# Kernel optimization log

Hardware: AMD Instinct MI355X
Metric: run time of the kernel (lower is better)

Reference implementation:

```python
import jax, jax.numpy as jnp
import numpy as np

INNER = 256   # inner_channel
NODES = 64    # nodes_num (prototypes)
EM_NUM = 3
DIAG_C = 128  # hardcoded diag_channel in FullyConnectGCLayer


def setup_inputs() -> dict:
    key = jax.random.key(0)
    ks = jax.random.split(key, 16)
    b, c, w, h = 4, 1024, 64, 64
    f32 = jnp.float32
    d = {}
    d["x"] = jax.random.normal(ks[0], (b, c, w, h), f32)
    # Conv2d weights re-initialized to N(0, 0.001) in Intra_graph.__init__
    d["W_in"] = 0.001 * jax.random.normal(ks[1], (INNER, c), f32)
    d["b_in"] = jnp.zeros((INNER,), f32)
    d["multi_proto"] = 0.001 * jax.random.normal(ks[2], (1, INNER, NODES), f32)
    d["pi0"] = jnp.ones((1, NODES), f32) / NODES
    # Conv1d layers keep default kaiming-uniform-ish init
    lim = 1.0 / np.sqrt(INNER)
    d["W_adj"] = jax.random.uniform(ks[3], (DIAG_C, INNER), f32, -lim, lim)
    d["b_adj"] = jax.random.uniform(ks[4], (DIAG_C,), f32, -lim, lim)
    d["W_diag"] = jax.random.uniform(ks[5], (DIAG_C, INNER), f32, -lim, lim)
    d["b_diag"] = jax.random.uniform(ks[6], (DIAG_C,), f32, -lim, lim)
    d["gcn_weight"] = 0.01 * jax.random.normal(ks[7], (INNER, INNER), f32)
    d["W_out"] = 0.001 * jax.random.normal(ks[8], (c, INNER), f32)
    d["b_out"] = jnp.zeros((c,), f32)
    d["gamma"] = jnp.ones((c,), f32)
    d["beta"] = jnp.zeros((c,), f32)
    d["W_out2"] = 0.001 * jax.random.normal(ks[9], (c, INNER), f32)
    d["b_out2"] = jnp.zeros((c,), f32)
    d["gamma2"] = jnp.ones((c,), f32)
    d["beta2"] = jnp.zeros((c,), f32)
    d["flag"] = 0
    return d


def _bn(y, g, bt):
    # BatchNorm2d in training mode: batch stats over (N,H,W), biased var, eps=1e-5
    m = jnp.mean(y, (0, 2, 3), keepdims=True)
    v = jnp.var(y, (0, 2, 3), keepdims=True)
    return (y - m) * jax.lax.rsqrt(v + 1e-5) * g[None, :, None, None] + bt[None, :, None, None]


def _forward(x, W_in, b_in, multi_proto, pi0, W_adj, b_adj, W_diag, b_diag,
             gcn_weight, W_out, b_out, gamma, beta, W_out2, b_out2, gamma2, beta2):
    b, c, w, h = x.shape
    wh = w * h
    x1 = (jnp.einsum('oi,bihw->bohw', W_in, x) + b_in[None, :, None, None]).reshape(b, INNER, wh)
    # ---- EM soft-clustering loop (runs under no_grad in torch) ----
    x1s = jax.lax.stop_gradient(x1)
    mu = jnp.broadcast_to(multi_proto, (b, INNER, NODES))
    pi = jnp.broadcast_to(pi0[None, :, :], (b, 1, NODES))
    for _ in range(EM_NUM):
        lik = jnp.einsum('bcm,bcn->bmn', x1s, mu)              # [b, wh, n]
        lik = jnp.exp(lik - jnp.max(lik, 2, keepdims=True))
        post = lik * pi
        post = post / (1e-18 + jnp.sum(post, 2, keepdims=True))
        prob = post / (1e-18 + jnp.sum(post, 1, keepdims=True))
        mu = jnp.einsum('bcm,bmn->bcn', x1s, prob)
        pi = jnp.sum(post, 1, keepdims=True) / wh
    post = jax.lax.stop_gradient(post)
    prob = jax.lax.stop_gradient(prob)
    # ---- aggregate to prototypes (grad flows through x1 only) ----
    x2 = jnp.einsum('bcm,bmn->bcn', x1, prob)                   # [b, inner, n]
    # ---- branch 2: scatter back, conv, bn ----
    x4 = jnp.einsum('bcn,bmn->bcm', x2, post).reshape(b, INNER, w, h)
    x4 = _bn(jnp.einsum('oi,bihw->bohw', W_out2, x4) + b_out2[None, :, None, None], gamma2, beta2)
    output2 = jax.nn.relu(jax.nn.relu(x4) + x)
    # ---- FullyConnectGCLayer on x2 ----
    xd = jnp.einsum('oi,bin->bon', W_diag, x2) + b_diag[None, :, None]
    dvec = jax.nn.sigmoid(jnp.mean(xd, 2))                      # [b, 128]
    xa = jnp.einsum('oi,bin->bon', W_adj, x2) + b_adj[None, :, None]  # [b, 128, n]
    # sigmoid(diag(d)) has 0.5 off-diagonal, sigmoid(d) on diagonal:
    # xa^T S xa = 0.5 * (1^T xa)^T (1^T xa) + xa^T diag(sig(d)-0.5) xa
    u = jnp.sum(xa, 1)                                          # [b, n]
    A = 0.5 * u[:, :, None] * u[:, None, :] + jnp.einsum('bcn,bc,bcm->bnm', xa, dvec - 0.5, xa)
    A = jax.nn.relu(A) + jnp.eye(NODES, dtype=x.dtype)[None]
    deg = jax.lax.stop_gradient(jnp.sum(A, 1) ** -0.5)          # no_grad degree, [b, n]
    A = deg[:, :, None] * A * deg[:, None, :]
    gout = jnp.einsum('oi,bin->bon', gcn_weight, jnp.einsum('bcn,bnm->bcm', x2, A))
    x2g = jax.nn.relu(gout) + x2                                # res_connect
    # ---- branch 1: scatter back, conv, bn ----
    x3 = jnp.einsum('bcn,bmn->bcm', x2g, post).reshape(b, INNER, w, h)
    x3 = _bn(jnp.einsum('oi,bihw->bohw', W_out, x3) + b_out[None, :, None, None], gamma, beta)
    output = jax.nn.relu(jax.nn.relu(x3) + x)
    return output, output2


def reference(x, W_in, b_in, multi_proto, pi0, W_adj, b_adj, W_diag, b_diag,
              gcn_weight, W_out, b_out, gamma, beta, W_out2, b_out2, gamma2, beta2, flag):
    # flag only gates a buffer EMA update (no effect on forward outputs)
    return _forward(x, W_in, b_in, multi_proto, pi0, W_adj, b_adj, W_diag, b_diag,
                    gcn_weight, W_out, b_out, gamma, beta, W_out2, b_out2, gamma2, beta2)
```

## Files before the change

kernel.cpp:

```cpp
#include <hip/hip_runtime.h>
#include <math.h>


typedef unsigned short u16;
typedef short s16x8 __attribute__((ext_vector_type(8)));
typedef float f32x4 __attribute__((ext_vector_type(4)));

constexpr int BB  = 4;
constexpr int CH  = 1024;
constexpr int IN  = 256;
constexpr int ND  = 64;
constexpr int WH  = 4096;
constexpr int DCN = 128;
constexpr size_t TOT = (size_t)BB * CH * WH;

__device__ inline u16 f2bf(float f) {
  unsigned u = __float_as_uint(f);
  return (u16)((u + 0x7fffu + ((u >> 16) & 1u)) >> 16);
}
__device__ inline s16x8 ld8(const u16* p) { return *(const s16x8*)p; }
#define MFMA16(a, b, c) __builtin_amdgcn_mfma_f32_16x16x32_bf16(a, b, c, 0, 0, 0)

__global__ void k_init(const float* __restrict__ Win, const float* __restrict__ mp,
                       const float* __restrict__ pi0, u16* __restrict__ Winb,
                       u16* __restrict__ mu_t, float* __restrict__ piw,
                       float* __restrict__ sp) {
  int idx = blockIdx.x * 256 + threadIdx.x;
  if (idx < IN * CH) { Winb[idx] = f2bf(Win[idx]); return; }
  int j = idx - IN * CH;
  if (j < BB * ND * IN) {
    int bb = j >> 14, n = (j >> 8) & 63, c = j & 255;
    mu_t[((size_t)(bb * ND + n)) * IN + c] = f2bf(mp[c * ND + n]);
    return;
  }
  j -= BB * ND * IN;
  if (j < BB * ND) { piw[j] = pi0[j & 63]; return; }
  j -= BB * ND;
  if (j < 3 * BB * ND) sp[j] = 0.f;
}

__global__ __launch_bounds__(512) void k_x1(
    const float* __restrict__ x, const u16* __restrict__ Winb,
    const float* __restrict__ bin, u16* __restrict__ x1, u16* __restrict__ x1t) {
  __shared__ u16 lt[64][40];
  const int t = threadIdx.x, w = t >> 6, lr = t & 15, lg = (t >> 4) & 3;
  const int wc = w & 3, wm = w >> 2;
  const int m0 = blockIdx.x * 64, b = blockIdx.y;
  const int si = t >> 4, sm = (t & 15) * 4;
  const float* xb = x + (size_t)b * CH * WH + m0 + sm;
  f32x4 acc[4][2];
#pragma unroll
  for (int i = 0; i < 4; ++i)
#pragma unroll
    for (int j = 0; j < 2; ++j) acc[i][j] = (f32x4){0.f, 0.f, 0.f, 0.f};
  const u16* wp = Winb + (size_t)(wc * 64 + lr) * CH + lg * 8;

  float4 nxt = *(const float4*)&xb[(size_t)si * WH];
  for (int k0 = 0; k0 < CH; k0 += 32) {
    float4 cur = nxt;
    __syncthreads();
    lt[sm + 0][si] = f2bf(cur.x); lt[sm + 1][si] = f2bf(cur.y);
    lt[sm + 2][si] = f2bf(cur.z); lt[sm + 3][si] = f2bf(cur.w);
    if (k0 + 32 < CH) nxt = *(const float4*)&xb[(size_t)(k0 + 32 + si) * WH];
    __syncthreads();
    s16x8 af[4], bf[2];
#pragma unroll
    for (int i = 0; i < 4; ++i) af[i] = ld8(wp + (size_t)i * 16 * CH + k0);
#pragma unroll
    for (int j = 0; j < 2; ++j) bf[j] = *(const s16x8*)&lt[wm * 32 + j * 16 + lr][lg * 8];
#pragma unroll
    for (int i = 0; i < 4; ++i)
#pragma unroll
      for (int j = 0; j < 2; ++j) acc[i][j] = MFMA16(af[i], bf[j], acc[i][j]);
  }
#pragma unroll
  for (int i = 0; i < 4; ++i) {
    const int cb = wc * 64 + i * 16 + lg * 4;
    const float4 bi = *(const float4*)&bin[cb];
    const float bia[4] = {bi.x, bi.y, bi.z, bi.w};
#pragma unroll
    for (int j = 0; j < 2; ++j) {
      const int m = m0 + wm * 32 + j * 16 + lr;
      float v[4];
#pragma unroll
      for (int r = 0; r < 4; ++r) v[r] = acc[i][j][r] + bia[r];
      ushort4 o;
      o.x = f2bf(v[0]); o.y = f2bf(v[1]); o.z = f2bf(v[2]); o.w = f2bf(v[3]);
      *(ushort4*)&x1t[((size_t)b * WH + m) * IN + cb] = o;
#pragma unroll
      for (int r = 0; r < 4; ++r)
        x1[((size_t)b * IN + cb + r) * WH + m] = f2bf(v[r]);
    }
  }
}

__global__ __launch_bounds__(256) void k_em(
    const u16* __restrict__ x1, const u16* __restrict__ x1t,
    const u16* __restrict__ mu_t, const float* __restrict__ piw,
    float* __restrict__ sp, u16* __restrict__ pmn,
    float* __restrict__ mup, float* __restrict__ gp, int doG) {
  __shared__ u16 ptl[64][72];
  const int t = threadIdx.x, w = t >> 6, lr = t & 15, lg = (t >> 4) & 3;
  const int mch = blockIdx.x, b = blockIdx.y;
  {
    f32x4 acc[4];
#pragma unroll
    for (int f = 0; f < 4; ++f) acc[f] = (f32x4){0.f, 0.f, 0.f, 0.f};
    const u16* ap = x1t + ((size_t)b * WH + mch * 64 + w * 16 + lr) * IN + lg * 8;
    const u16* bp = mu_t + ((size_t)b * ND + lr) * IN + lg * 8;
#pragma unroll
    for (int k0 = 0; k0 < IN; k0 += 32) {
      s16x8 a = ld8(ap + k0);
#pragma unroll
      for (int f = 0; f < 4; ++f)
        acc[f] = MFMA16(a, ld8(bp + f * 16 * IN + k0), acc[f]);
    }
    float pi_[4], spart[4] = {0.f, 0.f, 0.f, 0.f};
#pragma unroll
    for (int f = 0; f < 4; ++f) pi_[f] = piw[b * ND + f * 16 + lr];
#pragma unroll
    for (int r = 0; r < 4; ++r) {
      float v0 = acc[0][r], v1 = acc[1][r], v2 = acc[2][r], v3 = acc[3][r];
      float mx = fmaxf(fmaxf(v0, v1), fmaxf(v2, v3));
      mx = fmaxf(mx, __shfl_xor(mx, 1)); mx = fmaxf(mx, __shfl_xor(mx, 2));
      mx = fmaxf(mx, __shfl_xor(mx, 4)); mx = fmaxf(mx, __shfl_xor(mx, 8));
      float e0 = __expf(v0 - mx) * pi_[0], e1 = __expf(v1 - mx) * pi_[1];
      float e2 = __expf(v2 - mx) * pi_[2], e3 = __expf(v3 - mx) * pi_[3];
      float s = e0 + e1 + e2 + e3;
      s += __shfl_xor(s, 1); s += __shfl_xor(s, 2);
      s += __shfl_xor(s, 4); s += __shfl_xor(s, 8);
      const float inv = 1.f / (1e-18f + s);
      e0 *= inv; e1 *= inv; e2 *= inv; e3 *= inv;
      const int mloc = w * 16 + lg * 4 + r;
      const size_t gbase = ((size_t)b * WH + mch * 64 + mloc) * ND + lr;
      u16 q0 = f2bf(e0), q1 = f2bf(e1), q2 = f2bf(e2), q3 = f2bf(e3);
      pmn[gbase + 0]  = q0; pmn[gbase + 16] = q1;
      pmn[gbase + 32] = q2; pmn[gbase + 48] = q3;
      ptl[0 + lr][mloc]  = q0; ptl[16 + lr][mloc] = q1;
      ptl[32 + lr][mloc] = q2; ptl[48 + lr][mloc] = q3;
      spart[0] += e0; spart[1] += e1; spart[2] += e2; spart[3] += e3;
    }
#pragma unroll
    for (int f = 0; f < 4; ++f) {
      spart[f] += __shfl_xor(spart[f], 16);
      spart[f] += __shfl_xor(spart[f], 32);
    }
    if (((t >> 4) & 3) == 0) {
#pragma unroll
      for (int f = 0; f < 4; ++f)
        atomicAdd(&sp[b * ND + f * 16 + lr], spart[f]);
    }
  }
  __syncthreads();
  {
    f32x4 acc[4][4];
#pragma unroll
    for (int i = 0; i < 4; ++i)
#pragma unroll
      for (int j = 0; j < 4; ++j) acc[i][j] = (f32x4){0.f, 0.f, 0.f, 0.f};
    const u16* ap = x1 + ((size_t)b * IN + w * 64 + lr) * WH + mch * 64 + lg * 8;
#pragma unroll
    for (int ks = 0; ks < 2; ++ks) {
      s16x8 af[4], bf[4];
#pragma unroll
      for (int i = 0; i < 4; ++i) af[i] = ld8(ap + (size_t)i * 16 * WH + ks * 32);
#pragma unroll
      for (int j = 0; j < 4; ++j)
        bf[j] = *(const s16x8*)&ptl[j * 16 + lr][ks * 32 + lg * 8];
#pragma unroll
      for (int i = 0; i < 4; ++i)
#pragma unroll
        for (int j = 0; j < 4; ++j) acc[i][j] = MFMA16(af[i], bf[j], acc[i][j]);
    }
    float* mo = mup + ((size_t)mch * BB + b) * (IN * ND);
#pragma unroll
    for (int i = 0; i < 4; ++i)
#pragma unroll
      for (int j = 0; j < 4; ++j)
#pragma unroll
        for (int r = 0; r < 4; ++r) {
          const int c = w * 64 + i * 16 + lg * 4 + r, n = j * 16 + lr;
          mo[c * ND + n] = acc[i][j][r];
        }
  }
  if (doG) {
    f32x4 acc[4];
#pragma unroll
    for (int j = 0; j < 4; ++j) acc[j] = (f32x4){0.f, 0.f, 0.f, 0.f};
#pragma unroll
    for (int ks = 0; ks < 2; ++ks) {
      s16x8 a = *(const s16x8*)&ptl[w * 16 + lr][ks * 32 + lg * 8];
#pragma unroll
      for (int j = 0; j < 4; ++j) {
        s16x8 bq = *(const s16x8*)&ptl[j * 16 + lr][ks * 32 + lg * 8];
        acc[j] = MFMA16(a, bq, acc[j]);
      }
    }
    float* go = gp + ((size_t)mch * BB + b) * (ND * ND);
#pragma unroll
    for (int j = 0; j < 4; ++j)
#pragma unroll
      for (int r = 0; r < 4; ++r) {
        const int n1 = w * 16 + lg * 4 + r, n2 = j * 16 + lr;
        go[n1 * ND + n2] = acc[j][r];
      }
  }
}

__global__ void k_mu_red(const float* __restrict__ mup, const float* __restrict__ spb,
                         float* __restrict__ piw, float* __restrict__ mu,
                         u16* __restrict__ mu_t, const float* __restrict__ gp,
                         float* __restrict__ G, int doG) {
  const int idx = blockIdx.x * 256 + threadIdx.x;
  const int bb = idx >> 14, c = (idx >> 6) & 255, n = idx & 63;
  float s = 0.f;
#pragma unroll 8
  for (int ch = 0; ch < 64; ++ch)
    s += mup[((size_t)ch * BB + bb) * (IN * ND) + (idx & 16383)];
  const float v = s / (1e-18f + spb[bb * ND + n]);
  mu[idx] = v;
  mu_t[((size_t)(bb * ND + n)) * IN + c] = f2bf(v);
  if (idx < BB * ND) piw[idx] = spb[idx] * (1.f / (float)WH);
  if (doG && idx < BB * ND * ND) {
    float g = 0.f;
#pragma unroll 8
    for (int ch = 0; ch < 64; ++ch) g += gp[(size_t)ch * (BB * ND * ND) + idx];
    G[idx] = g;
  }
}

__global__ __launch_bounds__(256) void k_gcA(
    const float* __restrict__ mu, const float* __restrict__ gw,
    const float* __restrict__ Wa, const float* __restrict__ ba,
    const float* __restrict__ Wd, const float* __restrict__ bd,
    float* __restrict__ qbuf, float* __restrict__ xabuf, float* __restrict__ dv) {
  __shared__ float sx2[IN * ND];
  __shared__ float srm[IN];
  const int t = threadIdx.x, blk = blockIdx.x, b = blockIdx.y;
  if (blk < 6) {
    const float* src = mu + (size_t)b * IN * ND;
#pragma unroll
    for (int q4 = 0; q4 < 16; ++q4)
      *(float4*)&sx2[q4 * 1024 + t * 4] = *(const float4*)&src[q4 * 1024 + t * 4];
    __syncthreads();
    const int rg = t >> 4, cg = t & 15;
    const float* W = (blk < 4) ? gw + (size_t)(blk * 64 + rg * 4) * IN
                               : Wa + (size_t)((blk - 4) * 64 + rg * 4) * IN;
    float acc[4][4] = {};
    for (int i4 = 0; i4 < 64; ++i4) {
      float4 xv[4];
#pragma unroll
      for (int e = 0; e < 4; ++e)
        xv[e] = *(const float4*)&sx2[(i4 * 4 + e) * 64 + cg * 4];
#pragma unroll
      for (int rr = 0; rr < 4; ++rr) {
        const float4 w4 = *(const float4*)&W[(size_t)rr * IN + i4 * 4];
        acc[rr][0] += w4.x * xv[0].x + w4.y * xv[1].x + w4.z * xv[2].x + w4.w * xv[3].x;
        acc[rr][1] += w4.x * xv[0].y + w4.y * xv[1].y + w4.z * xv[2].y + w4.w * xv[3].y;
        acc[rr][2] += w4.x * xv[0].z + w4.y * xv[1].z + w4.z * xv[2].z + w4.w * xv[3].z;
        acc[rr][3] += w4.x * xv[0].w + w4.y * xv[1].w + w4.z * xv[2].w + w4.w * xv[3].w;
      }
    }
    if (blk < 4) {
      float* dst = qbuf + (size_t)b * IN * ND + (size_t)(blk * 64 + rg * 4) * ND + cg * 4;
#pragma unroll
      for (int rr = 0; rr < 4; ++rr)
        *(float4*)&dst[(size_t)rr * ND] =
            make_float4(acc[rr][0], acc[rr][1], acc[rr][2], acc[rr][3]);
    } else {
      const int xr = (blk - 4) * 64 + rg * 4;
      float* dst = xabuf + (size_t)b * DCN * ND + (size_t)xr * ND + cg * 4;
#pragma unroll
      for (int rr = 0; rr < 4; ++rr) {
        const float bv = ba[xr + rr];
        *(float4*)&dst[(size_t)rr * ND] =
            make_float4(acc[rr][0] + bv, acc[rr][1] + bv, acc[rr][2] + bv, acc[rr][3] + bv);
      }
    }
  } else {
    {
      const float* row = mu + (size_t)b * IN * ND + (size_t)t * ND;
      float s = 0.f;
#pragma unroll
      for (int n4 = 0; n4 < 16; ++n4) {
        float4 v = *(const float4*)&row[n4 * 4];
        s += v.x + v.y + v.z + v.w;
      }
      srm[t] = s * (1.f / ND);
    }
    __syncthreads();
    if (t < DCN) {
      float a = 0.f;
#pragma unroll
      for (int i4 = 0; i4 < 64; ++i4) {
        float4 w4 = *(const float4*)&Wd[(size_t)t * IN + i4 * 4];
        float4 r4 = *(const float4*)&srm[i4 * 4];
        a += w4.x * r4.x + w4.y * r4.y + w4.z * r4.z + w4.w * r4.w;
      }
      a += bd[t];
      dv[b * DCN + t] = 1.f / (1.f + __expf(-a)) - 0.5f;
    }
  }
}

__global__ __launch_bounds__(256) void k_gcB(
    const float* __restrict__ xabuf, const float* __restrict__ dv,
    float* __restrict__ ahat) {
  __shared__ float sxa[DCN * ND];
  __shared__ float sdv[DCN];
  __shared__ float su[ND];
  __shared__ float sdeg[ND];
  __shared__ float sA[ND * 65];
  const int t = threadIdx.x, b = blockIdx.x;
  const float* src = xabuf + (size_t)b * DCN * ND;
#pragma unroll
  for (int q4 = 0; q4 < 8; ++q4)
    *(float4*)&sxa[q4 * 1024 + t * 4] = *(const float4*)&src[q4 * 1024 + t * 4];
  if (t < DCN) sdv[t] = dv[b * DCN + t];
  __syncthreads();
  if (t < ND) {
    float s = 0.f;
    for (int dc = 0; dc < DCN; ++dc) s += sxa[dc * ND + t];
    su[t] = s;
  }
  __syncthreads();
  {
    const int n1g = t >> 4, n2g = t & 15;
    float acc[4][4] = {};
    for (int dc = 0; dc < DCN; ++dc) {
      const float dvv = sdv[dc];
      float4 v1 = *(const float4*)&sxa[dc * ND + n1g * 4];
      const float4 v2 = *(const float4*)&sxa[dc * ND + n2g * 4];
      v1.x *= dvv; v1.y *= dvv; v1.z *= dvv; v1.w *= dvv;
      acc[0][0] += v1.x * v2.x; acc[0][1] += v1.x * v2.y;
      acc[0][2] += v1.x * v2.z; acc[0][3] += v1.x * v2.w;
      acc[1][0] += v1.y * v2.x; acc[1][1] += v1.y * v2.y;
      acc[1][2] += v1.y * v2.z; acc[1][3] += v1.y * v2.w;
      acc[2][0] += v1.z * v2.x; acc[2][1] += v1.z * v2.y;
      acc[2][2] += v1.z * v2.z; acc[2][3] += v1.z * v2.w;
      acc[3][0] += v1.w * v2.x; acc[3][1] += v1.w * v2.y;
      acc[3][2] += v1.w * v2.z; acc[3][3] += v1.w * v2.w;
    }
#pragma unroll
    for (int i = 0; i < 4; ++i) {
      const int n1 = n1g * 4 + i;
      const float u1 = su[n1];
#pragma unroll
      for (int j = 0; j < 4; ++j) {
        const int n2 = n2g * 4 + j;
        const float v = acc[i][j] + 0.5f * u1 * su[n2];
        sA[n1 * 65 + n2] = fmaxf(v, 0.f) + (n1 == n2 ? 1.f : 0.f);
      }
    }
  }
  __syncthreads();
  if (t < ND) {
    float s = 0.f;
    for (int m = 0; m < ND; ++m) s += sA[m * 65 + t];
    sdeg[t] = rsqrtf(s);
  }
  __syncthreads();
  {
    const int n1g = t >> 4, n2g = t & 15;
#pragma unroll
    for (int i = 0; i < 4; ++i) {
      const int n1 = n1g * 4 + i;
      const float dr = sdeg[n1];
      float4 o;
      o.x = dr * sA[n1 * 65 + n2g * 4 + 0] * sdeg[n2g * 4 + 0];
      o.y = dr * sA[n1 * 65 + n2g * 4 + 1] * sdeg[n2g * 4 + 1];
      o.z = dr * sA[n1 * 65 + n2g * 4 + 2] * sdeg[n2g * 4 + 2];
      o.w = dr * sA[n1 * 65 + n2g * 4 + 3] * sdeg[n2g * 4 + 3];
      *(float4*)&ahat[(size_t)b * ND * ND + n1 * ND + n2g * 4] = o;
    }
  }
}

__global__ __launch_bounds__(256) void k_gcC(
    const float* __restrict__ qbuf, const float* __restrict__ ahat,
    const float* __restrict__ mu, float* __restrict__ x2g) {
  __shared__ float sq[64 * 68];
  __shared__ float sAh[64 * 65];
  const int t = threadIdx.x, ro = blockIdx.x * 64, b = blockIdx.y;
  {
    const int r = t >> 2, seg = (t & 3) * 16;
    const float* qs = qbuf + (size_t)b * IN * ND + (size_t)(ro + r) * ND + seg;
#pragma unroll
    for (int f = 0; f < 4; ++f) {
      float4 v = *(const float4*)&qs[f * 4];
      sq[r * 68 + seg + f * 4 + 0] = v.x; sq[r * 68 + seg + f * 4 + 1] = v.y;
      sq[r * 68 + seg + f * 4 + 2] = v.z; sq[r * 68 + seg + f * 4 + 3] = v.w;
    }
    const float* as = ahat + (size_t)b * ND * ND + (size_t)r * ND + seg;
#pragma unroll
    for (int f = 0; f < 4; ++f) {
      float4 v = *(const float4*)&as[f * 4];
      sAh[r * 65 + seg + f * 4 + 0] = v.x; sAh[r * 65 + seg + f * 4 + 1] = v.y;
      sAh[r * 65 + seg + f * 4 + 2] = v.z; sAh[r * 65 + seg + f * 4 + 3] = v.w;
    }
  }
  __syncthreads();
  const int rg = t >> 4, cg = t & 15;
  float acc[4][4] = {};
  for (int k = 0; k < ND; ++k) {
    const float4 a4 = *(const float4*)&sAh[k * 65 + cg * 4];
    float qv[4];
#pragma unroll
    for (int rr = 0; rr < 4; ++rr) qv[rr] = sq[(rg * 4 + rr) * 68 + k];
#pragma unroll
    for (int rr = 0; rr < 4; ++rr) {
      acc[rr][0] += qv[rr] * a4.x; acc[rr][1] += qv[rr] * a4.y;
      acc[rr][2] += qv[rr] * a4.z; acc[rr][3] += qv[rr] * a4.w;
    }
  }
#pragma unroll
  for (int rr = 0; rr < 4; ++rr) {
    const size_t off = (size_t)b * IN * ND + (size_t)(ro + rg * 4 + rr) * ND + cg * 4;
    const float4 xv = *(const float4*)&mu[off];
    float4 o;
    o.x = fmaxf(acc[rr][0], 0.f) + xv.x; o.y = fmaxf(acc[rr][1], 0.f) + xv.y;
    o.z = fmaxf(acc[rr][2], 0.f) + xv.z; o.w = fmaxf(acc[rr][3], 0.f) + xv.w;
    *(float4*)&x2g[off] = o;
  }
}

__global__ __launch_bounds__(256) void k_zdual(
    const float* __restrict__ Wo, const float* __restrict__ v1,
    float* __restrict__ z1o, u16* __restrict__ zb1o,
    const float* __restrict__ Wo2, const float* __restrict__ v2,
    float* __restrict__ z2o, u16* __restrict__ zb2o) {
  const float* W = blockIdx.z ? Wo2 : Wo;
  const float* v = blockIdx.z ? v2 : v1;
  float* z  = blockIdx.z ? z2o : z1o;
  u16* zb   = blockIdx.z ? zb2o : zb1o;
  __shared__ float As[16][68];
  __shared__ float Bs[16][64];
  const int t = threadIdx.x, tx = t & 15, ty = t >> 4;
  const int o0 = blockIdx.x * 64, bb = blockIdx.y;
  const int aoo = t >> 2, akq = (t & 3) * 4;
  const int bkk = t >> 4, bnq = (t & 15) * 4;
  float acc[4][4] = {};
  for (int k0 = 0; k0 < IN; k0 += 16) {
    {
      float4 w4 = *(const float4*)&W[(size_t)(o0 + aoo) * IN + k0 + akq];
      As[akq + 0][aoo] = w4.x; As[akq + 1][aoo] = w4.y;
      As[akq + 2][aoo] = w4.z; As[akq + 3][aoo] = w4.w;
    }
    *(float4*)&Bs[bkk][bnq] = *(const float4*)&v[((size_t)bb * IN + k0 + bkk) * ND + bnq];
    __syncthreads();
#pragma unroll
    for (int kk = 0; kk < 16; ++kk) {
      float4 a4 = *(const float4*)&As[kk][ty * 4];
      float4 b4 = *(const float4*)&Bs[kk][tx * 4];
      float ar[4] = {a4.x, a4.y, a4.z, a4.w}, br[4] = {b4.x, b4.y, b4.z, b4.w};
#pragma unroll
      for (int i = 0; i < 4; ++i)
#pragma unroll
        for (int j = 0; j < 4; ++j) acc[i][j] += ar[i] * br[j];
    }
    __syncthreads();
  }
#pragma unroll
  for (int i = 0; i < 4; ++i) {
    float4 r = make_float4(acc[i][0], acc[i][1], acc[i][2], acc[i][3]);
    const size_t off = ((size_t)bb * CH + o0 + ty * 4 + i) * ND + tx * 4;
    *(float4*)&z[off] = r;
    ushort4 h;
    h.x = f2bf(r.x); h.y = f2bf(r.y); h.z = f2bf(r.z); h.w = f2bf(r.w);
    *(ushort4*)&zb[off] = h;
  }
}

__global__ __launch_bounds__(256) void k_stats(
    const float* __restrict__ z1, const float* __restrict__ z2,
    const float* __restrict__ sp, const float* __restrict__ G,
    const float* __restrict__ gam, const float* __restrict__ bet,
    const float* __restrict__ gam2, const float* __restrict__ bet2,
    float* __restrict__ abc) {
  const int t = threadIdx.x;
  const int o = blockIdx.x * 4 + (t >> 6), lane = t & 63;
#pragma unroll
  for (int br = 0; br < 2; ++br) {
    const float* z = br ? z2 : z1;
    float macc = 0.f, eacc = 0.f;
    for (int bb = 0; bb < BB; ++bb) {
      const float zv = z[((size_t)bb * CH + o) * ND + lane];
      float s1 = zv * sp[bb * ND + lane];
      const float* Gb = G + (size_t)bb * ND * ND;
      float gz = 0.f;
      for (int k = 0; k < ND; ++k) {
        const float zk = __shfl(zv, k);
        gz += Gb[k * ND + lane] * zk;
      }
      float q = zv * gz;
#pragma unroll
      for (int off = 32; off; off >>= 1) {
        s1 += __shfl_xor(s1, off);
        q  += __shfl_xor(q, off);
      }
      macc += s1; eacc += q;
    }
    const float inv = 1.f / (float)((size_t)BB * WH);
    const float mean = macc * inv;
    const float var  = eacc * inv - mean * mean;
    const float a = (br ? gam2[o] : gam[o]) * rsqrtf(var + 1e-5f);
    const float c = (br ? bet2[o] : bet[o]) - mean * a;
    if (lane == 0) { abc[br * 2 * CH + o] = a; abc[br * 2 * CH + CH + o] = c; }
  }
}

__global__ __launch_bounds__(256) void k_epi(
    const u16* __restrict__ zb1, const u16* __restrict__ zb2,
    const u16* __restrict__ post, const float* __restrict__ abc,
    const float* __restrict__ x, float* __restrict__ out1, float* __restrict__ out2) {
  const int t = threadIdx.x, w = t >> 6, lr = t & 15, lg = (t >> 4) & 3;
  const int m0 = blockIdx.x * 256 + w * 64, o0 = blockIdx.y * 64, bb = blockIdx.z;
  f32x4 acc1[4][4], acc2[4][4];
#pragma unroll
  for (int i = 0; i < 4; ++i)
#pragma unroll
    for (int j = 0; j < 4; ++j) {
      acc1[i][j] = (f32x4){0.f, 0.f, 0.f, 0.f};
      acc2[i][j] = (f32x4){0.f, 0.f, 0.f, 0.f};
    }
  const u16* z1p = zb1 + ((size_t)bb * CH + o0 + lr) * ND + lg * 8;
  const u16* z2p = zb2 + ((size_t)bb * CH + o0 + lr) * ND + lg * 8;
  const u16* pp  = post + ((size_t)bb * WH + m0 + lr) * ND + lg * 8;
#pragma unroll
  for (int ks = 0; ks < 2; ++ks) {
    s16x8 a1[4], a2[4], bq[4];
#pragma unroll
    for (int i = 0; i < 4; ++i) {
      a1[i] = ld8(z1p + i * 16 * ND + ks * 32);
      a2[i] = ld8(z2p + i * 16 * ND + ks * 32);
    }
#pragma unroll
    for (int j = 0; j < 4; ++j) bq[j] = ld8(pp + j * 16 * ND + ks * 32);
#pragma unroll
    for (int i = 0; i < 4; ++i)
#pragma unroll
      for (int j = 0; j < 4; ++j) {
        acc1[i][j] = MFMA16(a1[i], bq[j], acc1[i][j]);
        acc2[i][j] = MFMA16(a2[i], bq[j], acc2[i][j]);
      }
  }
#pragma unroll
  for (int i = 0; i < 4; ++i)
#pragma unroll
    for (int r = 0; r < 4; ++r) {
      const int o = o0 + i * 16 + lg * 4 + r;
      const float a1v = abc[o], c1v = abc[CH + o];
      const float a2v = abc[2 * CH + o], c2v = abc[3 * CH + o];
      const size_t base = ((size_t)bb * CH + o) * WH + m0 + lr;
#pragma unroll
      for (int j = 0; j < 4; ++j) {
        const size_t off = base + j * 16;
        const float xv = x[off];
        out1[off] = fmaxf(fmaxf(a1v * acc1[i][j][r] + c1v, 0.f) + xv, 0.f);
        out2[off] = fmaxf(fmaxf(a2v * acc2[i][j][r] + c2v, 0.f) + xv, 0.f);
      }
    }
}

extern "C" void kernel_launch(void* const* d_in, const int* in_sizes, int n_in,
                              void* d_out, int out_size, void* d_ws, size_t ws_size,
                              hipStream_t stream) {
  (void)in_sizes; (void)n_in; (void)out_size; (void)ws_size;
  const float* x    = (const float*)d_in[0];
  const float* Win  = (const float*)d_in[1];
  const float* bin  = (const float*)d_in[2];
  const float* mp   = (const float*)d_in[3];
  const float* pi0  = (const float*)d_in[4];
  const float* Wa   = (const float*)d_in[5];
  const float* ba   = (const float*)d_in[6];
  const float* Wd   = (const float*)d_in[7];
  const float* bd   = (const float*)d_in[8];
  const float* gw   = (const float*)d_in[9];
  const float* Wo   = (const float*)d_in[10];
  const float* gam  = (const float*)d_in[12];
  const float* bet  = (const float*)d_in[13];
  const float* Wo2  = (const float*)d_in[14];
  const float* gam2 = (const float*)d_in[16];
  const float* bet2 = (const float*)d_in[17];

  char* ob = (char*)d_out;
  char* wp = (char*)d_ws;
  float* mup = (float*)(ob + 0);
  float* gp  = (float*)(ob + 16777216);
  float* z1  = (float*)(ob + 20971520);
  float* z2  = (float*)(ob + 22020096);
  u16*   x1    = (u16*)(wp + 0);
  u16*   x1t   = (u16*)(wp + 8388608);
  u16*   Winb  = (u16*)(wp + 16777216);
  u16*   mu_t  = (u16*)(wp + 17301504);
  u16*   pmn   = (u16*)(wp + 17432576);
  float* mu    = (float*)(wp + 19529728);
  float* x2g   = (float*)(wp + 19791872);
  u16*   zb1   = (u16*)(wp + 20054016);
  u16*   zb2   = (u16*)(wp + 20578304);
  float* sp3   = (float*)(wp + 21102592);
  float* piw   = (float*)(wp + 21105664);
  float* abc   = (float*)(wp + 21106688);
  float* G     = (float*)(wp + 21123072);
  float* qbuf  = (float*)(wp + 21188608);
  float* xabuf = (float*)(wp + 21450752);
  float* dvb   = (float*)(wp + 21581824);
  float* ahat  = (float*)(wp + 21583872);
  float* out1  = (float*)d_out;
  float* out2  = out1 + TOT;

  k_init<<<dim3(1284), 256, 0, stream>>>(Win, mp, pi0, Winb, mu_t, piw, sp3);
  k_x1<<<dim3(64, BB), 512, 0, stream>>>(x, Winb, bin, x1, x1t);
  for (int it = 0; it < 3; ++it) {
    float* spb = sp3 + it * 256;
    const int doG = (it == 2);
    k_em<<<dim3(64, BB), 256, 0, stream>>>(x1, x1t, mu_t, piw, spb, pmn, mup, gp, doG);
    k_mu_red<<<dim3(256), 256, 0, stream>>>(mup, spb, piw, mu, mu_t, gp, G, doG);
  }
  k_gcA<<<dim3(7, BB), 256, 0, stream>>>(mu, gw, Wa, ba, Wd, bd, qbuf, xabuf, dvb);
  k_gcB<<<dim3(BB), 256, 0, stream>>>(xabuf, dvb, ahat);
  k_gcC<<<dim3(4, BB), 256, 0, stream>>>(qbuf, ahat, mu, x2g);
  k_zdual<<<dim3(16, BB, 2), 256, 0, stream>>>(Wo, x2g, z1, zb1, Wo2, mu, z2, zb2);
  k_stats<<<dim3(256), 256, 0, stream>>>(z1, z2, sp3 + 512, G, gam, bet, gam2, bet2, abc);
  k_epi<<<dim3(16, 16, BB), 256, 0, stream>>>(zb1, zb2, pmn, abc, x, out1, out2);
}
```

Before: 232.9 us.

## Fuse EM iterations and graph stages into one cooperative persistent kernel

Replaces the eleven small kernel launches (three EM/reduce pairs, the three graph-conv stages, the dual output projection and the BN stats) with a single cooperative kernel of 256 blocks that separates stages with grid-wide syncs. It also runs the independent z2 projection alongside the graph-conv stage so that work overlaps. The aim is to remove launch gaps and the idle time of tiny kernels. In exchange, grid.sync adds its own cost, many blocks sit idle during the small stages, and the 65KB of shared memory per block limits how many blocks can be resident at once.

```diff
diff --git a/kernel.cpp b/kernel.cpp
--- a/kernel.cpp
+++ b/kernel.cpp
@@ -1,5 +1,8 @@
 #include <hip/hip_runtime.h>
+#include <hip/hip_cooperative_groups.h>
 #include <math.h>
+
+namespace cg = cooperative_groups;
 
 
 typedef unsigned short u16;
@@ -94,349 +97,24 @@
   }
 }
 
-__global__ __launch_bounds__(256) void k_em(
-    const u16* __restrict__ x1, const u16* __restrict__ x1t,
-    const u16* __restrict__ mu_t, const float* __restrict__ piw,
-    float* __restrict__ sp, u16* __restrict__ pmn,
-    float* __restrict__ mup, float* __restrict__ gp, int doG) {
-  __shared__ u16 ptl[64][72];
-  const int t = threadIdx.x, w = t >> 6, lr = t & 15, lg = (t >> 4) & 3;
-  const int mch = blockIdx.x, b = blockIdx.y;
-  {
-    f32x4 acc[4];
-#pragma unroll
-    for (int f = 0; f < 4; ++f) acc[f] = (f32x4){0.f, 0.f, 0.f, 0.f};
-    const u16* ap = x1t + ((size_t)b * WH + mch * 64 + w * 16 + lr) * IN + lg * 8;
-    const u16* bp = mu_t + ((size_t)b * ND + lr) * IN + lg * 8;
-#pragma unroll
-    for (int k0 = 0; k0 < IN; k0 += 32) {
-      s16x8 a = ld8(ap + k0);
-#pragma unroll
-      for (int f = 0; f < 4; ++f)
-        acc[f] = MFMA16(a, ld8(bp + f * 16 * IN + k0), acc[f]);
-    }
-    float pi_[4], spart[4] = {0.f, 0.f, 0.f, 0.f};
-#pragma unroll
-    for (int f = 0; f < 4; ++f) pi_[f] = piw[b * ND + f * 16 + lr];
-#pragma unroll
-    for (int r = 0; r < 4; ++r) {
-      float v0 = acc[0][r], v1 = acc[1][r], v2 = acc[2][r], v3 = acc[3][r];
-      float mx = fmaxf(fmaxf(v0, v1), fmaxf(v2, v3));
-      mx = fmaxf(mx, __shfl_xor(mx, 1)); mx = fmaxf(mx, __shfl_xor(mx, 2));
-      mx = fmaxf(mx, __shfl_xor(mx, 4)); mx = fmaxf(mx, __shfl_xor(mx, 8));
-      float e0 = __expf(v0 - mx) * pi_[0], e1 = __expf(v1 - mx) * pi_[1];
-      float e2 = __expf(v2 - mx) * pi_[2], e3 = __expf(v3 - mx) * pi_[3];
-      float s = e0 + e1 + e2 + e3;
-      s += __shfl_xor(s, 1); s += __shfl_xor(s, 2);
-      s += __shfl_xor(s, 4); s += __shfl_xor(s, 8);
-      const float inv = 1.f / (1e-18f + s);
-      e0 *= inv; e1 *= inv; e2 *= inv; e3 *= inv;
-      const int mloc = w * 16 + lg * 4 + r;
-      const size_t gbase = ((size_t)b * WH + mch * 64 + mloc) * ND + lr;
-      u16 q0 = f2bf(e0), q1 = f2bf(e1), q2 = f2bf(e2), q3 = f2bf(e3);
-      pmn[gbase + 0]  = q0; pmn[gbase + 16] = q1;
-      pmn[gbase + 32] = q2; pmn[gbase + 48] = q3;
-      ptl[0 + lr][mloc]  = q0; ptl[16 + lr][mloc] = q1;
-      ptl[32 + lr][mloc] = q2; ptl[48 + lr][mloc] = q3;
-      spart[0] += e0; spart[1] += e1; spart[2] += e2; spart[3] += e3;
-    }
-#pragma unroll
-    for (int f = 0; f < 4; ++f) {
-      spart[f] += __shfl_xor(spart[f], 16);
-      spart[f] += __shfl_xor(spart[f], 32);
-    }
-    if (((t >> 4) & 3) == 0) {
-#pragma unroll
-      for (int f = 0; f < 4; ++f)
-        atomicAdd(&sp[b * ND + f * 16 + lr], spart[f]);
-    }
-  }
-  __syncthreads();
-  {
-    f32x4 acc[4][4];
-#pragma unroll
-    for (int i = 0; i < 4; ++i)
-#pragma unroll
-      for (int j = 0; j < 4; ++j) acc[i][j] = (f32x4){0.f, 0.f, 0.f, 0.f};
-    const u16* ap = x1 + ((size_t)b * IN + w * 64 + lr) * WH + mch * 64 + lg * 8;
-#pragma unroll
-    for (int ks = 0; ks < 2; ++ks) {
-      s16x8 af[4], bf[4];
-#pragma unroll
-      for (int i = 0; i < 4; ++i) af[i] = ld8(ap + (size_t)i * 16 * WH + ks * 32);
-#pragma unroll
-      for (int j = 0; j < 4; ++j)
-        bf[j] = *(const s16x8*)&ptl[j * 16 + lr][ks * 32 + lg * 8];
-#pragma unroll
-      for (int i = 0; i < 4; ++i)
-#pragma unroll
-        for (int j = 0; j < 4; ++j) acc[i][j] = MFMA16(af[i], bf[j], acc[i][j]);
-    }
-    float* mo = mup + ((size_t)mch * BB + b) * (IN * ND);
-#pragma unroll
-    for (int i = 0; i < 4; ++i)
-#pragma unroll
-      for (int j = 0; j < 4; ++j)
-#pragma unroll
-        for (int r = 0; r < 4; ++r) {
-          const int c = w * 64 + i * 16 + lg * 4 + r, n = j * 16 + lr;
-          mo[c * ND + n] = acc[i][j][r];
-        }
-  }
-  if (doG) {
-    f32x4 acc[4];
-#pragma unroll
-    for (int j = 0; j < 4; ++j) acc[j] = (f32x4){0.f, 0.f, 0.f, 0.f};
-#pragma unroll
-    for (int ks = 0; ks < 2; ++ks) {
-      s16x8 a = *(const s16x8*)&ptl[w * 16 + lr][ks * 32 + lg * 8];
-#pragma unroll
-      for (int j = 0; j < 4; ++j) {
-        s16x8 bq = *(const s16x8*)&ptl[j * 16 + lr][ks * 32 + lg * 8];
-        acc[j] = MFMA16(a, bq, acc[j]);
-      }
-    }
-    float* go = gp + ((size_t)mch * BB + b) * (ND * ND);
-#pragma unroll
-    for (int j = 0; j < 4; ++j)
-#pragma unroll
-      for (int r = 0; r < 4; ++r) {
-        const int n1 = w * 16 + lg * 4 + r, n2 = j * 16 + lr;
-        go[n1 * ND + n2] = acc[j][r];
-      }
-  }
-}
-
-__global__ void k_mu_red(const float* __restrict__ mup, const float* __restrict__ spb,
-                         float* __restrict__ piw, float* __restrict__ mu,
-                         u16* __restrict__ mu_t, const float* __restrict__ gp,
-                         float* __restrict__ G, int doG) {
-  const int idx = blockIdx.x * 256 + threadIdx.x;
-  const int bb = idx >> 14, c = (idx >> 6) & 255, n = idx & 63;
-  float s = 0.f;
-#pragma unroll 8
-  for (int ch = 0; ch < 64; ++ch)
-    s += mup[((size_t)ch * BB + bb) * (IN * ND) + (idx & 16383)];
-  const float v = s / (1e-18f + spb[bb * ND + n]);
-  mu[idx] = v;
-  mu_t[((size_t)(bb * ND + n)) * IN + c] = f2bf(v);
-  if (idx < BB * ND) piw[idx] = spb[idx] * (1.f / (float)WH);
-  if (doG && idx < BB * ND * ND) {
-    float g = 0.f;
-#pragma unroll 8
-    for (int ch = 0; ch < 64; ++ch) g += gp[(size_t)ch * (BB * ND * ND) + idx];
-    G[idx] = g;
-  }
-}
-
-__global__ __launch_bounds__(256) void k_gcA(
-    const float* __restrict__ mu, const float* __restrict__ gw,
-    const float* __restrict__ Wa, const float* __restrict__ ba,
-    const float* __restrict__ Wd, const float* __restrict__ bd,
-    float* __restrict__ qbuf, float* __restrict__ xabuf, float* __restrict__ dv) {
-  __shared__ float sx2[IN * ND];
-  __shared__ float srm[IN];
-  const int t = threadIdx.x, blk = blockIdx.x, b = blockIdx.y;
-  if (blk < 6) {
-    const float* src = mu + (size_t)b * IN * ND;
-#pragma unroll
-    for (int q4 = 0; q4 < 16; ++q4)
-      *(float4*)&sx2[q4 * 1024 + t * 4] = *(const float4*)&src[q4 * 1024 + t * 4];
-    __syncthreads();
-    const int rg = t >> 4, cg = t & 15;
-    const float* W = (blk < 4) ? gw + (size_t)(blk * 64 + rg * 4) * IN
-                               : Wa + (size_t)((blk - 4) * 64 + rg * 4) * IN;
-    float acc[4][4] = {};
-    for (int i4 = 0; i4 < 64; ++i4) {
-      float4 xv[4];
-#pragma unroll
-      for (int e = 0; e < 4; ++e)
-        xv[e] = *(const float4*)&sx2[(i4 * 4 + e) * 64 + cg * 4];
-#pragma unroll
-      for (int rr = 0; rr < 4; ++rr) {
-        const float4 w4 = *(const float4*)&W[(size_t)rr * IN + i4 * 4];
-        acc[rr][0] += w4.x * xv[0].x + w4.y * xv[1].x + w4.z * xv[2].x + w4.w * xv[3].x;
-        acc[rr][1] += w4.x * xv[0].y + w4.y * xv[1].y + w4.z * xv[2].y + w4.w * xv[3].y;
-        acc[rr][2] += w4.x * xv[0].z + w4.y * xv[1].z + w4.z * xv[2].z + w4.w * xv[3].z;
-        acc[rr][3] += w4.x * xv[0].w + w4.y * xv[1].w + w4.z * xv[2].w + w4.w * xv[3].w;
-      }
-    }
-    if (blk < 4) {
-      float* dst = qbuf + (size_t)b * IN * ND + (size_t)(blk * 64 + rg * 4) * ND + cg * 4;
-#pragma unroll
-      for (int rr = 0; rr < 4; ++rr)
-        *(float4*)&dst[(size_t)rr * ND] =
-            make_float4(acc[rr][0], acc[rr][1], acc[rr][2], acc[rr][3]);
-    } else {
-      const int xr = (blk - 4) * 64 + rg * 4;
-      float* dst = xabuf + (size_t)b * DCN * ND + (size_t)xr * ND + cg * 4;
-#pragma unroll
-      for (int rr = 0; rr < 4; ++rr) {
-        const float bv = ba[xr + rr];
-        *(float4*)&dst[(size_t)rr * ND] =
-            make_float4(acc[rr][0] + bv, acc[rr][1] + bv, acc[rr][2] + bv, acc[rr][3] + bv);
-      }
-    }
-  } else {
-    {
-      const float* row = mu + (size_t)b * IN * ND + (size_t)t * ND;
-      float s = 0.f;
-#pragma unroll
-      for (int n4 = 0; n4 < 16; ++n4) {
-        float4 v = *(const float4*)&row[n4 * 4];
-        s += v.x + v.y + v.z + v.w;
-      }
-      srm[t] = s * (1.f / ND);
-    }
-    __syncthreads();
-    if (t < DCN) {
-      float a = 0.f;
-#pragma unroll
-      for (int i4 = 0; i4 < 64; ++i4) {
-        float4 w4 = *(const float4*)&Wd[(size_t)t * IN + i4 * 4];
-        float4 r4 = *(const float4*)&srm[i4 * 4];
-        a += w4.x * r4.x + w4.y * r4.y + w4.z * r4.z + w4.w * r4.w;
-      }
-      a += bd[t];
-      dv[b * DCN + t] = 1.f / (1.f + __expf(-a)) - 0.5f;
-    }
-  }
-}
-
-__global__ __launch_bounds__(256) void k_gcB(
-    const float* __restrict__ xabuf, const float* __restrict__ dv,
-    float* __restrict__ ahat) {
-  __shared__ float sxa[DCN * ND];
-  __shared__ float sdv[DCN];
-  __shared__ float su[ND];
-  __shared__ float sdeg[ND];
-  __shared__ float sA[ND * 65];
-  const int t = threadIdx.x, b = blockIdx.x;
-  const float* src = xabuf + (size_t)b * DCN * ND;
-#pragma unroll
-  for (int q4 = 0; q4 < 8; ++q4)
-    *(float4*)&sxa[q4 * 1024 + t * 4] = *(const float4*)&src[q4 * 1024 + t * 4];
-  if (t < DCN) sdv[t] = dv[b * DCN + t];
-  __syncthreads();
-  if (t < ND) {
-    float s = 0.f;
-    for (int dc = 0; dc < DCN; ++dc) s += sxa[dc * ND + t];
-    su[t] = s;
-  }
-  __syncthreads();
-  {
-    const int n1g = t >> 4, n2g = t & 15;
-    float acc[4][4] = {};
-    for (int dc = 0; dc < DCN; ++dc) {
-      const float dvv = sdv[dc];
-      float4 v1 = *(const float4*)&sxa[dc * ND + n1g * 4];
-      const float4 v2 = *(const float4*)&sxa[dc * ND + n2g * 4];
-      v1.x *= dvv; v1.y *= dvv; v1.z *= dvv; v1.w *= dvv;
-      acc[0][0] += v1.x * v2.x; acc[0][1] += v1.x * v2.y;
-      acc[0][2] += v1.x * v2.z; acc[0][3] += v1.x * v2.w;
-      acc[1][0] += v1.y * v2.x; acc[1][1] += v1.y * v2.y;
-      acc[1][2] += v1.y * v2.z; acc[1][3] += v1.y * v2.w;
-      acc[2][0] += v1.z * v2.x; acc[2][1] += v1.z * v2.y;
-      acc[2][2] += v1.z * v2.z; acc[2][3] += v1.z * v2.w;
-      acc[3][0] += v1.w * v2.x; acc[3][1] += v1.w * v2.y;
-      acc[3][2] += v1.w * v2.z; acc[3][3] += v1.w * v2.w;
-    }
-#pragma unroll
-    for (int i = 0; i < 4; ++i) {
-      const int n1 = n1g * 4 + i;
-      const float u1 = su[n1];
-#pragma unroll
-      for (int j = 0; j < 4; ++j) {
-        const int n2 = n2g * 4 + j;
-        const float v = acc[i][j] + 0.5f * u1 * su[n2];
-        sA[n1 * 65 + n2] = fmaxf(v, 0.f) + (n1 == n2 ? 1.f : 0.f);
-      }
-    }
-  }
-  __syncthreads();
-  if (t < ND) {
-    float s = 0.f;
-    for (int m = 0; m < ND; ++m) s += sA[m * 65 + t];
-    sdeg[t] = rsqrtf(s);
-  }
-  __syncthreads();
-  {
-    const int n1g = t >> 4, n2g = t & 15;
-#pragma unroll
-    for (int i = 0; i < 4; ++i) {
-      const int n1 = n1g * 4 + i;
-      const float dr = sdeg[n1];
-      float4 o;
-      o.x = dr * sA[n1 * 65 + n2g * 4 + 0] * sdeg[n2g * 4 + 0];
-      o.y = dr * sA[n1 * 65 + n2g * 4 + 1] * sdeg[n2g * 4 + 1];
-      o.z = dr * sA[n1 * 65 + n2g * 4 + 2] * sdeg[n2g * 4 + 2];
-      o.w = dr * sA[n1 * 65 + n2g * 4 + 3] * sdeg[n2g * 4 + 3];
-      *(float4*)&ahat[(size_t)b * ND * ND + n1 * ND + n2g * 4] = o;
-    }
-  }
-}
-
-__global__ __launch_bounds__(256) void k_gcC(
-    const float* __restrict__ qbuf, const float* __restrict__ ahat,
-    const float* __restrict__ mu, float* __restrict__ x2g) {
-  __shared__ float sq[64 * 68];
-  __shared__ float sAh[64 * 65];
-  const int t = threadIdx.x, ro = blockIdx.x * 64, b = blockIdx.y;
-  {
-    const int r = t >> 2, seg = (t & 3) * 16;
-    const float* qs = qbuf + (size_t)b * IN * ND + (size_t)(ro + r) * ND + seg;
-#pragma unroll
-    for (int f = 0; f < 4; ++f) {
-      float4 v = *(const float4*)&qs[f * 4];
-      sq[r * 68 + seg + f * 4 + 0] = v.x; sq[r * 68 + seg + f * 4 + 1] = v.y;
-      sq[r * 68 + seg + f * 4 + 2] = v.z; sq[r * 68 + seg + f * 4 + 3] = v.w;
-    }
-    const float* as = ahat + (size_t)b * ND * ND + (size_t)r * ND + seg;
-#pragma unroll
-    for (int f = 0; f < 4; ++f) {
-      float4 v = *(const float4*)&as[f * 4];
-      sAh[r * 65 + seg + f * 4 + 0] = v.x; sAh[r * 65 + seg + f * 4 + 1] = v.y;
-      sAh[r * 65 + seg + f * 4 + 2] = v.z; sAh[r * 65 + seg + f * 4 + 3] = v.w;
-    }
-  }
-  __syncthreads();
-  const int rg = t >> 4, cg = t & 15;
-  float acc[4][4] = {};
-  for (int k = 0; k < ND; ++k) {
-    const float4 a4 = *(const float4*)&sAh[k * 65 + cg * 4];
-    float qv[4];
-#pragma unroll
-    for (int rr = 0; rr < 4; ++rr) qv[rr] = sq[(rg * 4 + rr) * 68 + k];
-#pragma unroll
-    for (int rr = 0; rr < 4; ++rr) {
-      acc[rr][0] += qv[rr] * a4.x; acc[rr][1] += qv[rr] * a4.y;
-      acc[rr][2] += qv[rr] * a4.z; acc[rr][3] += qv[rr] * a4.w;
-    }
-  }
-#pragma unroll
-  for (int rr = 0; rr < 4; ++rr) {
-    const size_t off = (size_t)b * IN * ND + (size_t)(ro + rg * 4 + rr) * ND + cg * 4;
-    const float4 xv = *(const float4*)&mu[off];
-    float4 o;
-    o.x = fmaxf(acc[rr][0], 0.f) + xv.x; o.y = fmaxf(acc[rr][1], 0.f) + xv.y;
-    o.z = fmaxf(acc[rr][2], 0.f) + xv.z; o.w = fmaxf(acc[rr][3], 0.f) + xv.w;
-    *(float4*)&x2g[off] = o;
-  }
-}
-
-__global__ __launch_bounds__(256) void k_zdual(
-    const float* __restrict__ Wo, const float* __restrict__ v1,
-    float* __restrict__ z1o, u16* __restrict__ zb1o,
-    const float* __restrict__ Wo2, const float* __restrict__ v2,
-    float* __restrict__ z2o, u16* __restrict__ zb2o) {
-  const float* W = blockIdx.z ? Wo2 : Wo;
-  const float* v = blockIdx.z ? v2 : v1;
-  float* z  = blockIdx.z ? z2o : z1o;
-  u16* zb   = blockIdx.z ? zb2o : zb1o;
-  __shared__ float As[16][68];
-  __shared__ float Bs[16][64];
-  const int t = threadIdx.x, tx = t & 15, ty = t >> 4;
-  const int o0 = blockIdx.x * 64, bb = blockIdx.y;
+struct MidArgs {
+  const u16* x1; const u16* x1t; u16* mu_t; float* piw; float* sp3;
+  u16* pmn; float* mup; float* gp; float* G; float* mu;
+  const float* gw; const float* Wa; const float* ba;
+  const float* Wd; const float* bd;
+  float* qbuf; float* xabuf; float* dv; float* ahat; float* x2g;
+  const float* Wo; const float* Wo2; float* z1; float* z2;
+  u16* zb1; u16* zb2;
+  const float* gam; const float* bet; const float* gam2; const float* bet2;
+  float* abc;
+};
+
+__device__ void zdual_body(const float* __restrict__ W, const float* __restrict__ v,
+                           float* __restrict__ z, u16* __restrict__ zb,
+                           int o0, int bb, int t, char* smem) {
+  float (*As)[68] = (float(*)[68])smem;
+  float (*Bs)[64] = (float(*)[64])(smem + 4352);
+  const int tx = t & 15, ty = t >> 4;
   const int aoo = t >> 2, akq = (t & 3) * 4;
   const int bkk = t >> 4, bnq = (t & 15) * 4;
   float acc[4][4] = {};
@@ -471,41 +149,371 @@
   }
 }
 
-__global__ __launch_bounds__(256) void k_stats(
-    const float* __restrict__ z1, const float* __restrict__ z2,
-    const float* __restrict__ sp, const float* __restrict__ G,
-    const float* __restrict__ gam, const float* __restrict__ bet,
-    const float* __restrict__ gam2, const float* __restrict__ bet2,
-    float* __restrict__ abc) {
-  const int t = threadIdx.x;
-  const int o = blockIdx.x * 4 + (t >> 6), lane = t & 63;
-#pragma unroll
-  for (int br = 0; br < 2; ++br) {
-    const float* z = br ? z2 : z1;
-    float macc = 0.f, eacc = 0.f;
-    for (int bb = 0; bb < BB; ++bb) {
-      const float zv = z[((size_t)bb * CH + o) * ND + lane];
-      float s1 = zv * sp[bb * ND + lane];
-      const float* Gb = G + (size_t)bb * ND * ND;
-      float gz = 0.f;
-      for (int k = 0; k < ND; ++k) {
-        const float zk = __shfl(zv, k);
-        gz += Gb[k * ND + lane] * zk;
-      }
-      float q = zv * gz;
-#pragma unroll
-      for (int off = 32; off; off >>= 1) {
-        s1 += __shfl_xor(s1, off);
-        q  += __shfl_xor(q, off);
-      }
-      macc += s1; eacc += q;
-    }
-    const float inv = 1.f / (float)((size_t)BB * WH);
-    const float mean = macc * inv;
-    const float var  = eacc * inv - mean * mean;
-    const float a = (br ? gam2[o] : gam[o]) * rsqrtf(var + 1e-5f);
-    const float c = (br ? bet2[o] : bet[o]) - mean * a;
-    if (lane == 0) { abc[br * 2 * CH + o] = a; abc[br * 2 * CH + CH + o] = c; }
+__global__ __launch_bounds__(256) void k_mid(MidArgs a) {
+  __shared__ __align__(16) char smem[66560];
+  cg::grid_group grid = cg::this_grid();
+  const int t = threadIdx.x, bid = blockIdx.x;
+  const int w = t >> 6, lr = t & 15, lg = (t >> 4) & 3;
+
+  for (int it = 0; it < 3; ++it) {
+    float* spb = a.sp3 + it * 256;
+    const int doG = (it == 2);
+    const int mch = bid & 63, b = bid >> 6;
+    u16 (*ptl)[72] = (u16(*)[72])smem;
+    {
+      f32x4 acc[4];
+#pragma unroll
+      for (int f = 0; f < 4; ++f) acc[f] = (f32x4){0.f, 0.f, 0.f, 0.f};
+      const u16* ap = a.x1t + ((size_t)b * WH + mch * 64 + w * 16 + lr) * IN + lg * 8;
+      const u16* bp = a.mu_t + ((size_t)b * ND + lr) * IN + lg * 8;
+#pragma unroll
+      for (int k0 = 0; k0 < IN; k0 += 32) {
+        s16x8 av = ld8(ap + k0);
+#pragma unroll
+        for (int f = 0; f < 4; ++f)
+          acc[f] = MFMA16(av, ld8(bp + f * 16 * IN + k0), acc[f]);
+      }
+      float pi_[4], spart[4] = {0.f, 0.f, 0.f, 0.f};
+#pragma unroll
+      for (int f = 0; f < 4; ++f) pi_[f] = a.piw[b * ND + f * 16 + lr];
+#pragma unroll
+      for (int r = 0; r < 4; ++r) {
+        float v0 = acc[0][r], v1 = acc[1][r], v2 = acc[2][r], v3 = acc[3][r];
+        float mx = fmaxf(fmaxf(v0, v1), fmaxf(v2, v3));
+        mx = fmaxf(mx, __shfl_xor(mx, 1)); mx = fmaxf(mx, __shfl_xor(mx, 2));
+        mx = fmaxf(mx, __shfl_xor(mx, 4)); mx = fmaxf(mx, __shfl_xor(mx, 8));
+        float e0 = __expf(v0 - mx) * pi_[0], e1 = __expf(v1 - mx) * pi_[1];
+        float e2 = __expf(v2 - mx) * pi_[2], e3 = __expf(v3 - mx) * pi_[3];
+        float s = e0 + e1 + e2 + e3;
+        s += __shfl_xor(s, 1); s += __shfl_xor(s, 2);
+        s += __shfl_xor(s, 4); s += __shfl_xor(s, 8);
+        const float inv = 1.f / (1e-18f + s);
+        e0 *= inv; e1 *= inv; e2 *= inv; e3 *= inv;
+        const int mloc = w * 16 + lg * 4 + r;
+        const size_t gbase = ((size_t)b * WH + mch * 64 + mloc) * ND + lr;
+        u16 q0 = f2bf(e0), q1 = f2bf(e1), q2 = f2bf(e2), q3 = f2bf(e3);
+        a.pmn[gbase + 0]  = q0; a.pmn[gbase + 16] = q1;
+        a.pmn[gbase + 32] = q2; a.pmn[gbase + 48] = q3;
+        ptl[0 + lr][mloc]  = q0; ptl[16 + lr][mloc] = q1;
+        ptl[32 + lr][mloc] = q2; ptl[48 + lr][mloc] = q3;
+        spart[0] += e0; spart[1] += e1; spart[2] += e2; spart[3] += e3;
+      }
+#pragma unroll
+      for (int f = 0; f < 4; ++f) {
+        spart[f] += __shfl_xor(spart[f], 16);
+        spart[f] += __shfl_xor(spart[f], 32);
+      }
+      if (((t >> 4) & 3) == 0) {
+#pragma unroll
+        for (int f = 0; f < 4; ++f)
+          atomicAdd(&spb[b * ND + f * 16 + lr], spart[f]);
+      }
+    }
+    __syncthreads();
+    {
+      f32x4 acc[4][4];
+#pragma unroll
+      for (int i = 0; i < 4; ++i)
+#pragma unroll
+        for (int j = 0; j < 4; ++j) acc[i][j] = (f32x4){0.f, 0.f, 0.f, 0.f};
+      const u16* ap = a.x1 + ((size_t)b * IN + w * 64 + lr) * WH + mch * 64 + lg * 8;
+#pragma unroll
+      for (int ks = 0; ks < 2; ++ks) {
+        s16x8 af[4], bf[4];
+#pragma unroll
+        for (int i = 0; i < 4; ++i) af[i] = ld8(ap + (size_t)i * 16 * WH + ks * 32);
+#pragma unroll
+        for (int j = 0; j < 4; ++j)
+          bf[j] = *(const s16x8*)&ptl[j * 16 + lr][ks * 32 + lg * 8];
+#pragma unroll
+        for (int i = 0; i < 4; ++i)
+#pragma unroll
+          for (int j = 0; j < 4; ++j) acc[i][j] = MFMA16(af[i], bf[j], acc[i][j]);
+      }
+      float* mo = a.mup + ((size_t)mch * BB + b) * (IN * ND);
+#pragma unroll
+      for (int i = 0; i < 4; ++i)
+#pragma unroll
+        for (int j = 0; j < 4; ++j)
+#pragma unroll
+          for (int r = 0; r < 4; ++r) {
+            const int c = w * 64 + i * 16 + lg * 4 + r, n = j * 16 + lr;
+            mo[c * ND + n] = acc[i][j][r];
+          }
+    }
+    if (doG) {
+      f32x4 acc[4];
+#pragma unroll
+      for (int j = 0; j < 4; ++j) acc[j] = (f32x4){0.f, 0.f, 0.f, 0.f};
+#pragma unroll
+      for (int ks = 0; ks < 2; ++ks) {
+        s16x8 av = *(const s16x8*)&ptl[w * 16 + lr][ks * 32 + lg * 8];
+#pragma unroll
+        for (int j = 0; j < 4; ++j) {
+          s16x8 bq = *(const s16x8*)&ptl[j * 16 + lr][ks * 32 + lg * 8];
+          acc[j] = MFMA16(av, bq, acc[j]);
+        }
+      }
+      float* go = a.gp + ((size_t)mch * BB + b) * (ND * ND);
+#pragma unroll
+      for (int j = 0; j < 4; ++j)
+#pragma unroll
+        for (int r = 0; r < 4; ++r) {
+          const int n1 = w * 16 + lg * 4 + r, n2 = j * 16 + lr;
+          go[n1 * ND + n2] = acc[j][r];
+        }
+    }
+    grid.sync();
+    {
+      const int idx = bid * 256 + t;
+      const int bb = idx >> 14, c = (idx >> 6) & 255, n = idx & 63;
+      float s = 0.f;
+#pragma unroll 8
+      for (int ch = 0; ch < 64; ++ch)
+        s += a.mup[((size_t)ch * BB + bb) * (IN * ND) + (idx & 16383)];
+      const float v = s / (1e-18f + spb[bb * ND + n]);
+      a.mu[idx] = v;
+      a.mu_t[((size_t)(bb * ND + n)) * IN + c] = f2bf(v);
+      if (idx < BB * ND) a.piw[idx] = spb[idx] * (1.f / (float)WH);
+      if (doG && idx < BB * ND * ND) {
+        float g = 0.f;
+#pragma unroll 8
+        for (int ch = 0; ch < 64; ++ch) g += a.gp[(size_t)ch * (BB * ND * ND) + idx];
+        a.G[idx] = g;
+      }
+    }
+    grid.sync();
+  }
+
+  if (bid < 28) {
+    const int blk = bid % 7, b = bid / 7;
+    float* sx2 = (float*)smem;
+    float* srm = (float*)(smem + 65536);
+    if (blk < 6) {
+      const float* src = a.mu + (size_t)b * IN * ND;
+#pragma unroll
+      for (int q4 = 0; q4 < 16; ++q4)
+        *(float4*)&sx2[q4 * 1024 + t * 4] = *(const float4*)&src[q4 * 1024 + t * 4];
+      __syncthreads();
+      const int rg = t >> 4, cg2 = t & 15;
+      const float* W = (blk < 4) ? a.gw + (size_t)(blk * 64 + rg * 4) * IN
+                                 : a.Wa + (size_t)((blk - 4) * 64 + rg * 4) * IN;
+      float acc[4][4] = {};
+      for (int i4 = 0; i4 < 64; ++i4) {
+        float4 xv[4];
+#pragma unroll
+        for (int e = 0; e < 4; ++e)
+          xv[e] = *(const float4*)&sx2[(i4 * 4 + e) * 64 + cg2 * 4];
+#pragma unroll
+        for (int rr = 0; rr < 4; ++rr) {
+          const float4 w4 = *(const float4*)&W[(size_t)rr * IN + i4 * 4];
+          acc[rr][0] += w4.x * xv[0].x + w4.y * xv[1].x + w4.z * xv[2].x + w4.w * xv[3].x;
+          acc[rr][1] += w4.x * xv[0].y + w4.y * xv[1].y + w4.z * xv[2].y + w4.w * xv[3].y;
+          acc[rr][2] += w4.x * xv[0].z + w4.y * xv[1].z + w4.z * xv[2].z + w4.w * xv[3].z;
+          acc[rr][3] += w4.x * xv[0].w + w4.y * xv[1].w + w4.z * xv[2].w + w4.w * xv[3].w;
+        }
+      }
+      if (blk < 4) {
+        float* dst = a.qbuf + (size_t)b * IN * ND + (size_t)(blk * 64 + rg * 4) * ND + cg2 * 4;
+#pragma unroll
+        for (int rr = 0; rr < 4; ++rr)
+          *(float4*)&dst[(size_t)rr * ND] =
+              make_float4(acc[rr][0], acc[rr][1], acc[rr][2], acc[rr][3]);
+      } else {
+        const int xr = (blk - 4) * 64 + rg * 4;
+        float* dst = a.xabuf + (size_t)b * DCN * ND + (size_t)xr * ND + cg2 * 4;
+#pragma unroll
+        for (int rr = 0; rr < 4; ++rr) {
+          const float bv = a.ba[xr + rr];
+          *(float4*)&dst[(size_t)rr * ND] =
+              make_float4(acc[rr][0] + bv, acc[rr][1] + bv, acc[rr][2] + bv, acc[rr][3] + bv);
+        }
+      }
+    } else {
+      {
+        const float* row = a.mu + (size_t)b * IN * ND + (size_t)t * ND;
+        float s = 0.f;
+#pragma unroll
+        for (int n4 = 0; n4 < 16; ++n4) {
+          float4 v = *(const float4*)&row[n4 * 4];
+          s += v.x + v.y + v.z + v.w;
+        }
+        srm[t] = s * (1.f / ND);
+      }
+      __syncthreads();
+      if (t < DCN) {
+        float av = 0.f;
+#pragma unroll
+        for (int i4 = 0; i4 < 64; ++i4) {
+          float4 w4 = *(const float4*)&a.Wd[(size_t)t * IN + i4 * 4];
+          float4 r4 = *(const float4*)&srm[i4 * 4];
+          av += w4.x * r4.x + w4.y * r4.y + w4.z * r4.z + w4.w * r4.w;
+        }
+        av += a.bd[t];
+        a.dv[b * DCN + t] = 1.f / (1.f + __expf(-av)) - 0.5f;
+      }
+    }
+  } else if (bid >= 32 && bid < 96) {
+    const int zid = bid - 32;
+    zdual_body(a.Wo2, a.mu, a.z2, a.zb2, (zid & 15) * 64, zid >> 4, t, smem);
+  }
+  grid.sync();
+
+  if (bid < 4) {
+    const int b = bid;
+    float* sxa  = (float*)smem;
+    float* sA   = (float*)(smem + 32768);
+    float* sdv  = (float*)(smem + 49408);
+    float* su   = (float*)(smem + 49920);
+    float* sdeg = (float*)(smem + 50176);
+    const float* src = a.xabuf + (size_t)b * DCN * ND;
+#pragma unroll
+    for (int q4 = 0; q4 < 8; ++q4)
+      *(float4*)&sxa[q4 * 1024 + t * 4] = *(const float4*)&src[q4 * 1024 + t * 4];
+    if (t < DCN) sdv[t] = a.dv[b * DCN + t];
+    __syncthreads();
+    if (t < ND) {
+      float s = 0.f;
+      for (int dc = 0; dc < DCN; ++dc) s += sxa[dc * ND + t];
+      su[t] = s;
+    }
+    __syncthreads();
+    {
+      const int n1g = t >> 4, n2g = t & 15;
+      float acc[4][4] = {};
+      for (int dc = 0; dc < DCN; ++dc) {
+        const float dvv = sdv[dc];
+        float4 v1 = *(const float4*)&sxa[dc * ND + n1g * 4];
+        const float4 v2 = *(const float4*)&sxa[dc * ND + n2g * 4];
+        v1.x *= dvv; v1.y *= dvv; v1.z *= dvv; v1.w *= dvv;
+        acc[0][0] += v1.x * v2.x; acc[0][1] += v1.x * v2.y;
+        acc[0][2] += v1.x * v2.z; acc[0][3] += v1.x * v2.w;
+        acc[1][0] += v1.y * v2.x; acc[1][1] += v1.y * v2.y;
+        acc[1][2] += v1.y * v2.z; acc[1][3] += v1.y * v2.w;
+        acc[2][0] += v1.z * v2.x; acc[2][1] += v1.z * v2.y;
+        acc[2][2] += v1.z * v2.z; acc[2][3] += v1.z * v2.w;
+        acc[3][0] += v1.w * v2.x; acc[3][1] += v1.w * v2.y;
+        acc[3][2] += v1.w * v2.z; acc[3][3] += v1.w * v2.w;
+      }
+#pragma unroll
+      for (int i = 0; i < 4; ++i) {
+        const int n1 = n1g * 4 + i;
+        const float u1 = su[n1];
+#pragma unroll
+        for (int j = 0; j < 4; ++j) {
+          const int n2 = n2g * 4 + j;
+          const float v = acc[i][j] + 0.5f * u1 * su[n2];
+          sA[n1 * 65 + n2] = fmaxf(v, 0.f) + (n1 == n2 ? 1.f : 0.f);
+        }
+      }
+    }
+    __syncthreads();
+    if (t < ND) {
+      float s = 0.f;
+      for (int m = 0; m < ND; ++m) s += sA[m * 65 + t];
+      sdeg[t] = rsqrtf(s);
+    }
+    __syncthreads();
+    {
+      const int n1g = t >> 4, n2g = t & 15;
+#pragma unroll
+      for (int i = 0; i < 4; ++i) {
+        const int n1 = n1g * 4 + i;
+        const float dr = sdeg[n1];
+        float4 o;
+        o.x = dr * sA[n1 * 65 + n2g * 4 + 0] * sdeg[n2g * 4 + 0];
+        o.y = dr * sA[n1 * 65 + n2g * 4 + 1] * sdeg[n2g * 4 + 1];
+        o.z = dr * sA[n1 * 65 + n2g * 4 + 2] * sdeg[n2g * 4 + 2];
+        o.w = dr * sA[n1 * 65 + n2g * 4 + 3] * sdeg[n2g * 4 + 3];
+        *(float4*)&a.ahat[(size_t)b * ND * ND + n1 * ND + n2g * 4] = o;
+      }
+    }
+  }
+  grid.sync();
+
+  if (bid < 16) {
+    const int ro = (bid & 3) * 64, b = bid >> 2;
+    float* sq  = (float*)smem;
+    float* sAh = (float*)(smem + 17408);
+    {
+      const int r = t >> 2, seg = (t & 3) * 16;
+      const float* qs = a.qbuf + (size_t)b * IN * ND + (size_t)(ro + r) * ND + seg;
+#pragma unroll
+      for (int f = 0; f < 4; ++f) {
+        float4 v = *(const float4*)&qs[f * 4];
+        sq[r * 68 + seg + f * 4 + 0] = v.x; sq[r * 68 + seg + f * 4 + 1] = v.y;
+        sq[r * 68 + seg + f * 4 + 2] = v.z; sq[r * 68 + seg + f * 4 + 3] = v.w;
+      }
+      const float* as = a.ahat + (size_t)b * ND * ND + (size_t)r * ND + seg;
+#pragma unroll
+      for (int f = 0; f < 4; ++f) {
+        float4 v = *(const float4*)&as[f * 4];
+        sAh[r * 65 + seg + f * 4 + 0] = v.x; sAh[r * 65 + seg + f * 4 + 1] = v.y;
+        sAh[r * 65 + seg + f * 4 + 2] = v.z; sAh[r * 65 + seg + f * 4 + 3] = v.w;
+      }
+    }
+    __syncthreads();
+    const int rg = t >> 4, cg2 = t & 15;
+    float acc[4][4] = {};
+    for (int k = 0; k < ND; ++k) {
+      const float4 a4 = *(const float4*)&sAh[k * 65 + cg2 * 4];
+      float qv[4];
+#pragma unroll
+      for (int rr = 0; rr < 4; ++rr) qv[rr] = sq[(rg * 4 + rr) * 68 + k];
+#pragma unroll
+      for (int rr = 0; rr < 4; ++rr) {
+        acc[rr][0] += qv[rr] * a4.x; acc[rr][1] += qv[rr] * a4.y;
+        acc[rr][2] += qv[rr] * a4.z; acc[rr][3] += qv[rr] * a4.w;
+      }
+    }
+#pragma unroll
+    for (int rr = 0; rr < 4; ++rr) {
+      const size_t off = (size_t)b * IN * ND + (size_t)(ro + rg * 4 + rr) * ND + cg2 * 4;
+      const float4 xv = *(const float4*)&a.mu[off];
+      float4 o;
+      o.x = fmaxf(acc[rr][0], 0.f) + xv.x; o.y = fmaxf(acc[rr][1], 0.f) + xv.y;
+      o.z = fmaxf(acc[rr][2], 0.f) + xv.z; o.w = fmaxf(acc[rr][3], 0.f) + xv.w;
+      *(float4*)&a.x2g[off] = o;
+    }
+  }
+  grid.sync();
+
+  if (bid < 64) {
+    zdual_body(a.Wo, a.x2g, a.z1, a.zb1, (bid & 15) * 64, bid >> 4, t, smem);
+  }
+  grid.sync();
+
+  {
+    const float* spb = a.sp3 + 512;
+    const int o = bid * 4 + (t >> 6), lane = t & 63;
+#pragma unroll
+    for (int br = 0; br < 2; ++br) {
+      const float* z = br ? a.z2 : a.z1;
+      float macc = 0.f, eacc = 0.f;
+      for (int bb = 0; bb < BB; ++bb) {
+        const float zv = z[((size_t)bb * CH + o) * ND + lane];
+        float s1 = zv * spb[bb * ND + lane];
+        const float* Gb = a.G + (size_t)bb * ND * ND;
+        float gz = 0.f;
+        for (int k = 0; k < ND; ++k) {
+          const float zk = __shfl(zv, k);
+          gz += Gb[k * ND + lane] * zk;
+        }
+        float q = zv * gz;
+#pragma unroll
+        for (int off = 32; off; off >>= 1) {
+          s1 += __shfl_xor(s1, off);
+          q  += __shfl_xor(q, off);
+        }
+        macc += s1; eacc += q;
+      }
+      const float inv = 1.f / (float)((size_t)BB * WH);
+      const float mean = macc * inv;
+      const float var  = eacc * inv - mean * mean;
+      const float av = (br ? a.gam2[o] : a.gam[o]) * rsqrtf(var + 1e-5f);
+      const float cv = (br ? a.bet2[o] : a.bet[o]) - mean * av;
+      if (lane == 0) { a.abc[br * 2 * CH + o] = av; a.abc[br * 2 * CH + CH + o] = cv; }
+    }
   }
 }
 
@@ -611,16 +619,18 @@
 
   k_init<<<dim3(1284), 256, 0, stream>>>(Win, mp, pi0, Winb, mu_t, piw, sp3);
   k_x1<<<dim3(64, BB), 512, 0, stream>>>(x, Winb, bin, x1, x1t);
-  for (int it = 0; it < 3; ++it) {
-    float* spb = sp3 + it * 256;
-    const int doG = (it == 2);
-    k_em<<<dim3(64, BB), 256, 0, stream>>>(x1, x1t, mu_t, piw, spb, pmn, mup, gp, doG);
-    k_mu_red<<<dim3(256), 256, 0, stream>>>(mup, spb, piw, mu, mu_t, gp, G, doG);
-  }
-  k_gcA<<<dim3(7, BB), 256, 0, stream>>>(mu, gw, Wa, ba, Wd, bd, qbuf, xabuf, dvb);
-  k_gcB<<<dim3(BB), 256, 0, stream>>>(xabuf, dvb, ahat);
-  k_gcC<<<dim3(4, BB), 256, 0, stream>>>(qbuf, ahat, mu, x2g);
-  k_zdual<<<dim3(16, BB, 2), 256, 0, stream>>>(Wo, x2g, z1, zb1, Wo2, mu, z2, zb2);
-  k_stats<<<dim3(256), 256, 0, stream>>>(z1, z2, sp3 + 512, G, gam, bet, gam2, bet2, abc);
+
+  MidArgs ma;
+  ma.x1 = x1; ma.x1t = x1t; ma.mu_t = mu_t; ma.piw = piw; ma.sp3 = sp3;
+  ma.pmn = pmn; ma.mup = mup; ma.gp = gp; ma.G = G; ma.mu = mu;
+  ma.gw = gw; ma.Wa = Wa; ma.ba = ba; ma.Wd = Wd; ma.bd = bd;
+  ma.qbuf = qbuf; ma.xabuf = xabuf; ma.dv = dvb; ma.ahat = ahat; ma.x2g = x2g;
+  ma.Wo = Wo; ma.Wo2 = Wo2; ma.z1 = z1; ma.z2 = z2;
+  ma.zb1 = zb1; ma.zb2 = zb2;
+  ma.gam = gam; ma.bet = bet; ma.gam2 = gam2; ma.bet2 = bet2;
+  ma.abc = abc;
+  void* kargs[] = {&ma};
+  hipLaunchCooperativeKernel((void*)k_mid, dim3(256), dim3(256), kargs, 0, stream);
+
   k_epi<<<dim3(16, 16, BB), 256, 0, stream>>>(zb1, zb2, pmn, abc, x, out1, out2);
 }
```

Result: slower. 530.9 us (+128.0%).
